# Kernel tuning notes

Hardware: AMD Instinct MI355X
Metric: run time of the kernel (lower is better)

## Reference

```python
import jax, jax.numpy as jnp
import numpy as np
import math

LN_EPS = 1e-5

def layer_norm(x, g, b):
    mu = jnp.mean(x, axis=-1, keepdims=True)
    var = jnp.mean(jnp.square(x - mu), axis=-1, keepdims=True)
    return (x - mu) * jax.lax.rsqrt(var + LN_EPS) * g + b

def positional_encoding(seq_len, d_model):
    pos = jnp.arange(seq_len, dtype=jnp.float32)[:, None]
    div = jnp.exp(jnp.arange(0, d_model, 2, dtype=jnp.float32) * (-math.log(10000.0) / d_model))
    ang = pos * div  # [S, D/2]
    # interleave: even indices sin, odd indices cos
    return jnp.stack([jnp.sin(ang), jnp.cos(ang)], axis=-1).reshape(seq_len, d_model)

def setup_inputs() -> dict:
    key = jax.random.key(0)
    V, D, H, L, F, B, S = 32000, 768, 12, 6, 3072, 4, 1024
    ks = jax.random.split(key, 12)
    s = 0.02
    inp = {
        'tokens': jax.random.randint(ks[0], (B, S), 0, V),
        'emb': jax.random.normal(ks[1], (V, D), jnp.float32) * s,
        'Wq': jax.random.normal(ks[2], (L, D, D), jnp.float32) * s,
        'bq': jnp.zeros((L, D), jnp.float32),
        'Wk': jax.random.normal(ks[3], (L, D, D), jnp.float32) * s,
        'bk': jnp.zeros((L, D), jnp.float32),
        'Wv': jax.random.normal(ks[4], (L, D, D), jnp.float32) * s,
        'bv': jnp.zeros((L, D), jnp.float32),
        'Wo': jax.random.normal(ks[5], (L, D, D), jnp.float32) * s,
        'bo': jnp.zeros((L, D), jnp.float32),
        'W1': jax.random.normal(ks[6], (L, D, F), jnp.float32) * s,
        'b1': jnp.zeros((L, F), jnp.float32),
        'W2': jax.random.normal(ks[7], (L, F, D), jnp.float32) * s,
        'b2': jnp.zeros((L, D), jnp.float32),
        'ln1_g': jnp.ones((L, D), jnp.float32), 'ln1_b': jnp.zeros((L, D), jnp.float32),
        'ln2_g': jnp.ones((L, D), jnp.float32), 'ln2_b': jnp.zeros((L, D), jnp.float32),
        'lnf_g': jnp.ones((D,), jnp.float32), 'lnf_b': jnp.zeros((D,), jnp.float32),
        'head_W': jax.random.normal(ks[8], (V, D), jnp.float32) * s,
    }
    return inp

def gpt_forward(tokens, emb, Wq, bq, Wk, bk, Wv, bv, Wo, bo, W1, b1, W2, b2,
                ln1_g, ln1_b, ln2_g, ln2_b, lnf_g, lnf_b, head_W):
    B, S = tokens.shape
    D = emb.shape[1]
    H = 12
    dk = D // H
    scale = 1.0 / math.sqrt(dk)
    causal = jnp.tril(jnp.ones((S, S), dtype=bool))  # [S,S]

    x = emb[tokens] + positional_encoding(S, D)  # [B,S,D]

    def block(x, p):
        wq, bq_, wk, bk_, wv, bv_, wo, bo_, w1, b1_, w2, b2_, g1, be1, g2, be2 = p
        h = layer_norm(x, g1, be1)
        q = (h @ wq + bq_).reshape(B, S, H, dk)
        k = (h @ wk + bk_).reshape(B, S, H, dk)
        v = (h @ wv + bv_).reshape(B, S, H, dk)
        scores = jnp.einsum('bqhd,bkhd->bhqk', q, k) * scale
        scores = jnp.where(causal, scores, -jnp.inf)
        attn = jax.nn.softmax(scores, axis=-1)
        o = jnp.einsum('bhqk,bkhd->bqhd', attn, v).reshape(B, S, D)
        x = x + o @ wo + bo_
        h2 = layer_norm(x, g2, be2)
        ff = jax.nn.gelu(h2 @ w1 + b1_, approximate=False) @ w2 + b2_
        x = x + ff
        return x, None

    layer_params = (Wq, bq, Wk, bk, Wv, bv, Wo, bo, W1, b1, W2, b2,
                    ln1_g, ln1_b, ln2_g, ln2_b)
    x, _ = jax.lax.scan(block, x, layer_params)
    x = layer_norm(x, lnf_g, lnf_b)
    logits = jnp.einsum('bsd,vd->bsv', x, head_W)  # head bias=False
    return logits

def reference(tokens, emb, Wq, bq, Wk, bk, Wv, bv, Wo, bo, W1, b1, W2, b2,
              ln1_g, ln1_b, ln2_g, ln2_b, lnf_g, lnf_b, head_W):
    return gpt_forward(tokens, emb, Wq, bq, Wk, bk, Wv, bv, Wo, bo, W1, b1, W2, b2,
                       ln1_g, ln1_b, ln2_g, ln2_b, lnf_g, lnf_b, head_W)
```

## Files before the change

kernel.cpp:

```cpp
#include <hip/hip_runtime.h>
#include <hip/hip_bf16.h>
#include <math.h>

#define BB 4
#define SS 1024
#define DD 768
#define HH 12
#define LL 6
#define FF 3072
#define VV 32000
#define DK 64
#define MM (BB * SS)

typedef __attribute__((ext_vector_type(8))) short s8v;
typedef __attribute__((ext_vector_type(4))) float f4v;

__device__ inline unsigned short f2bf_bits(float f) {
    unsigned u = __builtin_bit_cast(unsigned, f);
    unsigned r = (u + 0x7fffu + ((u >> 16) & 1u)) >> 16;
    return (unsigned short)r;
}

__device__ inline void gl_lds16(const void* g, void* l) {
    __builtin_amdgcn_global_load_lds((const __attribute__((address_space(1))) void*)g,
                                     (__attribute__((address_space(3))) void*)l, 16, 0, 0);
}

__global__ void embed_kernel(const int* __restrict__ tokens,
                             const float* __restrict__ emb,
                             float* __restrict__ x) {
    const int row = blockIdx.x;
    const int s = row % SS;
    const int tok = tokens[row];
    const float* er = emb + (size_t)tok * DD;
    float* xr = x + (size_t)row * DD;
    const float neg_ln_base = -logf(10000.0f) / (float)DD;
    for (int d = threadIdx.x; d < DD; d += blockDim.x) {
        int i2 = d & ~1;
        float div = expf((float)i2 * neg_ln_base);
        float ang = (float)s * div;
        float pe = (d & 1) ? cosf(ang) : sinf(ang);
        xr[d] = er[d] + pe;
    }
}

template <int OUTBF>
__global__ __launch_bounds__(256) void ln_kernel(const float* __restrict__ x,
                                                 const float* __restrict__ g,
                                                 const float* __restrict__ b,
                                                 void* __restrict__ outp) {
    const int row = blockIdx.x;
    const float* xr = x + (size_t)row * DD;
    float s = 0.f, s2 = 0.f;
    for (int d = threadIdx.x; d < DD; d += blockDim.x) {
        float v = xr[d];
        s += v; s2 += v * v;
    }
    __shared__ float rs[4], rs2[4];
    for (int off = 32; off; off >>= 1) {
        s  += __shfl_down(s, off);
        s2 += __shfl_down(s2, off);
    }
    const int wid = threadIdx.x >> 6;
    if ((threadIdx.x & 63) == 0) { rs[wid] = s; rs2[wid] = s2; }
    __syncthreads();
    s  = rs[0] + rs[1] + rs[2] + rs[3];
    s2 = rs2[0] + rs2[1] + rs2[2] + rs2[3];
    const float mu = s / (float)DD;
    const float var = s2 / (float)DD - mu * mu;
    const float r = rsqrtf(var + 1e-5f);
    for (int d = threadIdx.x; d < DD; d += blockDim.x) {
        float v = (xr[d] - mu) * r * g[d] + b[d];
        if (OUTBF) ((unsigned short*)outp)[(size_t)row * DD + d] = f2bf_bits(v);
        else       ((float*)outp)[(size_t)row * DD + d] = v;
    }
}

__global__ __launch_bounds__(256) void prep_kernel(const float* __restrict__ Wq,
                                                   const float* __restrict__ Wk,
                                                   const float* __restrict__ Wv,
                                                   const float* __restrict__ Wo,
                                                   const float* __restrict__ W1,
                                                   const float* __restrict__ W2,
                                                   unsigned short* __restrict__ wqkvT,
                                                   unsigned short* __restrict__ woT,
                                                   unsigned short* __restrict__ w1T,
                                                   unsigned short* __restrict__ w2T) {
    const size_t DxD = (size_t)DD * DD, DxF = (size_t)DD * FF;
    const int lid = blockIdx.x / 1728;
    const int id  = blockIdx.x % 1728;
    const float* src; unsigned short* dst; int R, C, t;
    if (id < 432)       { int seg = id / 144; t = id % 144;
                          src = (seg == 0 ? Wq : seg == 1 ? Wk : Wv) + lid * DxD;
                          dst = wqkvT + lid * 3 * DxD + (size_t)seg * DxD; R = DD; C = DD; }
    else if (id < 576)  { t = id - 432; src = Wo + lid * DxD; dst = woT + lid * DxD; R = DD; C = DD; }
    else if (id < 1152) { t = id - 576;  src = W1 + lid * DxF; dst = w1T + lid * DxF; R = DD; C = FF; }
    else                { t = id - 1152; src = W2 + lid * DxF; dst = w2T + lid * DxF; R = FF; C = DD; }
    const int tilesC = C / 64;
    const int r0 = (t / tilesC) * 64, c0 = (t % tilesC) * 64;
    __shared__ float tb[64][65];
    const int lr = threadIdx.x >> 6, lc = threadIdx.x & 63;
    #pragma unroll
    for (int it = 0; it < 16; ++it) {
        int r = it * 4 + lr;
        tb[r][lc] = src[(size_t)(r0 + r) * C + c0 + lc];
    }
    __syncthreads();
    #pragma unroll
    for (int it = 0; it < 16; ++it) {
        int c = it * 4 + lr;
        dst[(size_t)(c0 + c) * R + r0 + lc] = f2bf_bits(tb[lc][c]);
    }
}

__global__ __launch_bounds__(256) void conv_kernel(const float* __restrict__ in,
                                                   unsigned short* __restrict__ out,
                                                   long n4) {
    long i = (long)blockIdx.x * 256 + threadIdx.x;
    if (i < n4) {
        float4 v = ((const float4*)in)[i];
        ushort4 o;
        o.x = f2bf_bits(v.x); o.y = f2bf_bits(v.y);
        o.z = f2bf_bits(v.z); o.w = f2bf_bits(v.w);
        ((ushort4*)out)[i] = o;
    }
}

template <int BM, int BN, int WGM, int WGN, int ACT, int RES, int OUTMODE>
__global__ __launch_bounds__(256) void gemm_mfma(const unsigned short* __restrict__ A,
                                                 const unsigned short* __restrict__ Bt,
                                                 const float* __restrict__ bias,
                                                 const float* res,
                                                 void* Cout, int M, int N, int K,
                                                 const float* biasK, const float* biasV,
                                                 unsigned short* kout, unsigned short* vtout) {
    __shared__ unsigned short As[BM * 32];
    __shared__ unsigned short Bs[BN * 32];
    constexpr int MF = (BM / WGM) / 16;
    constexpr int NF = (BN / WGN) / 16;
    const int tid = threadIdx.x;
    const int bm = blockIdx.y * BM, bn = blockIdx.x * BN;
    const int lane = tid & 63;
    const int wave = tid >> 6;
    const int wr = (wave / WGN) * (BM / WGM);
    const int wc = (wave % WGN) * (BN / WGN);

    f4v acc[MF][NF];
    #pragma unroll
    for (int i = 0; i < MF; i++)
        #pragma unroll
        for (int j = 0; j < NF; j++)
            acc[i][j] = (f4v){0.f, 0.f, 0.f, 0.f};

    const int arow = tid >> 2;
    const int acol = (tid & 3) * 8;
    const int fr = lane & 15;
    const int fk = (lane >> 4) * 8;

    for (int k0 = 0; k0 < K; k0 += 32) {
        #pragma unroll
        for (int i = 0; i < BM / 64; i++)
            gl_lds16(A + (size_t)(bm + i * 64 + arow) * K + k0 + acol,
                     (char*)As + i * 4096 + tid * 16);
        #pragma unroll
        for (int i = 0; i < BN / 64; i++)
            gl_lds16(Bt + (size_t)(bn + i * 64 + arow) * K + k0 + acol,
                     (char*)Bs + i * 4096 + tid * 16);
        __syncthreads();
        s8v af[MF], bf[NF];
        #pragma unroll
        for (int i = 0; i < MF; i++)
            af[i] = *(const s8v*)(As + (wr + i * 16 + fr) * 32 + fk);
        #pragma unroll
        for (int j = 0; j < NF; j++)
            bf[j] = *(const s8v*)(Bs + (wc + j * 16 + fr) * 32 + fk);
        #pragma unroll
        for (int i = 0; i < MF; i++)
            #pragma unroll
            for (int j = 0; j < NF; j++)
                acc[i][j] = __builtin_amdgcn_mfma_f32_16x16x32_bf16(af[i], bf[j], acc[i][j], 0, 0, 0);
        __syncthreads();
    }

    const int r0 = bm + wr + (lane >> 4) * 4;
    const int c0 = bn + wc + fr;
    #pragma unroll
    for (int i = 0; i < MF; i++) {
        const int rb = r0 + i * 16;
        #pragma unroll
        for (int j = 0; j < NF; j++) {
            const int c = c0 + j * 16;
            if (OUTMODE == 3) {
                const int seg = (c >= 1536) ? 2 : (c >= 768 ? 1 : 0);
                const int cc = c - seg * 768;
                const float bb = (seg == 0 ? bias[cc] : seg == 1 ? biasK[cc] : biasV[cc]);
                if (seg < 2) {
                    unsigned short* dst = (seg == 0 ? (unsigned short*)Cout : kout);
                    #pragma unroll
                    for (int q = 0; q < 4; q++)
                        dst[(size_t)(rb + q) * DD + cc] = f2bf_bits(acc[i][j][q] + bb);
                } else {
                    const int b_ = rb / SS, s_ = rb % SS;
                    const int h_ = cc >> 6, dd = cc & 63;
                    ushort4 pk;
                    pk.x = f2bf_bits(acc[i][j][0] + bb);
                    pk.y = f2bf_bits(acc[i][j][1] + bb);
                    pk.z = f2bf_bits(acc[i][j][2] + bb);
                    pk.w = f2bf_bits(acc[i][j][3] + bb);
                    *(ushort4*)(vtout + ((size_t)(b_ * HH + h_) * DK + dd) * SS + s_) = pk;
                }
            } else {
                const float bv = bias ? bias[c] : 0.f;
                #pragma unroll
                for (int q = 0; q < 4; q++) {
                    const int r = rb + q;
                    float v = acc[i][j][q] + bv;
                    if (ACT) v = 0.5f * v * (1.0f + erff(v * 0.70710678118654752f));
                    if (RES) v += res[(size_t)r * N + c];
                    if (OUTMODE == 1) ((unsigned short*)Cout)[(size_t)r * N + c] = f2bf_bits(v);
                    else              ((float*)Cout)[(size_t)r * N + c] = v;
                }
            }
        }
    }
}

__global__ __launch_bounds__(512) void gemm_head(const unsigned short* __restrict__ A,
                                                 const unsigned short* __restrict__ Bt,
                                                 float* __restrict__ C,
                                                 int M, int N, int K) {
    __shared__ unsigned short As[256 * 32];
    __shared__ unsigned short Bs[128 * 32];
    const int tid = threadIdx.x;

    const int f = blockIdx.y * gridDim.x + blockIdx.x;
    const int v = (f & 7) * 500 + (f >> 3);
    int bx, by;
    if (v < 3840) {
        const int bnd = v >> 8;
        const int r = v & 255;
        by = r >> 4;
        bx = bnd * 16 + (r & 15);
    } else {
        const int r = v - 3840;
        by = r / 10;
        bx = 240 + r % 10;
    }
    const int bm = by * 256, bn = bx * 128;

    const int lane = tid & 63;
    const int wave = tid >> 6;
    const int wm = (wave >> 1) * 64;
    const int wn = (wave & 1) * 64;

    f4v acc[4][4];
    #pragma unroll
    for (int i = 0; i < 4; i++)
        #pragma unroll
        for (int j = 0; j < 4; j++)
            acc[i][j] = (f4v){0.f, 0.f, 0.f, 0.f};

    const int arow = tid >> 2;
    const int acol = (tid & 3) * 8;
    const unsigned short* gA0 = A  + (size_t)(bm + arow) * K + acol;
    const unsigned short* gA1 = gA0 + (size_t)128 * K;
    const unsigned short* gB  = Bt + (size_t)(bn + arow) * K + acol;
    char* lA0 = (char*)As + tid * 16;
    char* lA1 = lA0 + 8192;
    char* lB  = (char*)Bs + tid * 16;

    const int fr = lane & 15;
    const int fk = (lane >> 4) * 8;

    for (int k0 = 0; k0 < K; k0 += 32) {
        gl_lds16(gA0 + k0, lA0);
        gl_lds16(gA1 + k0, lA1);
        gl_lds16(gB + k0, lB);
        __syncthreads();
        s8v af[4], bf[4];
        #pragma unroll
        for (int i = 0; i < 4; i++)
            af[i] = *(const s8v*)(As + (wm + i * 16 + fr) * 32 + fk);
        #pragma unroll
        for (int j = 0; j < 4; j++)
            bf[j] = *(const s8v*)(Bs + (wn + j * 16 + fr) * 32 + fk);
        #pragma unroll
        for (int i = 0; i < 4; i++)
            #pragma unroll
            for (int j = 0; j < 4; j++)
                acc[i][j] = __builtin_amdgcn_mfma_f32_16x16x32_bf16(af[i], bf[j], acc[i][j], 0, 0, 0);
        __syncthreads();
    }

    const int r0 = bm + wm + (lane >> 4) * 4;
    const int c0 = bn + wn + fr;
    #pragma unroll
    for (int i = 0; i < 4; i++) {
        #pragma unroll
        for (int j = 0; j < 4; j++) {
            const int c = c0 + j * 16;
            #pragma unroll
            for (int q = 0; q < 4; q++) {
                const int r = r0 + i * 16 + q;
                __builtin_nontemporal_store(acc[i][j][q], &C[(size_t)r * N + c]);
            }
        }
    }
}

__global__ __launch_bounds__(256) void fattn_kernel(const unsigned short* __restrict__ qb,
                                                    const unsigned short* __restrict__ kb,
                                                    const unsigned short* __restrict__ vt,
                                                    unsigned short* __restrict__ o) {
    __shared__ unsigned short Ks[128 * 64];
    __shared__ unsigned short Vs[64 * 128];
    __shared__ unsigned short Ps[4][16 * 128];

    const int qt = (int)gridDim.x - 1 - (int)blockIdx.x;
    const int bh = blockIdx.y;
    const int b = bh / HH, h = bh % HH;
    const int tid = threadIdx.x;
    const int lane = tid & 63;
    const int w = tid >> 6;
    const int fr = lane & 15;
    const int g  = lane >> 4;

    const int krow_ = tid >> 3;
    const int kcol = ((tid & 7) ^ (krow_ & 7)) * 8;
    const int vrow_ = tid >> 4;
    const int vcol = ((tid & 15) ^ (vrow_ & 7)) * 8;

    const int q0w = qt * 64 + w * 16;
    s8v qf[2];
    {
        const unsigned short* qrow = qb + (size_t)(b * SS + q0w + fr) * DD + h * DK + g * 8;
        qf[0] = *(const s8v*)(qrow);
        qf[1] = *(const s8v*)(qrow + 32);
    }

    f4v ofr[4];
    #pragma unroll
    for (int dj = 0; dj < 4; dj++) ofr[dj] = (f4v){0.f, 0.f, 0.f, 0.f};
    float mrow[4] = {-1e30f, -1e30f, -1e30f, -1e30f};
    float lrow[4] = {0.f, 0.f, 0.f, 0.f};

    unsigned short* Pw = &Ps[w][0];
    const int ktiles = qt / 2 + 1;

    for (int t = 0; t < ktiles; ++t) {
        const int k0 = t * 128;
        #pragma unroll
        for (int i = 0; i < 4; i++) {
            const int r = i * 32 + krow_;
            gl_lds16(kb + (size_t)(b * SS + k0 + r) * DD + h * DK + kcol,
                     (char*)Ks + i * 4096 + tid * 16);
        }
        #pragma unroll
        for (int i = 0; i < 4; i++) {
            const int d = i * 16 + vrow_;
            gl_lds16(vt + ((size_t)bh * DK + d) * SS + k0 + vcol,
                     (char*)Vs + i * 4096 + tid * 16);
        }
        __syncthreads();

        const bool diag = (t == ktiles - 1);
        float p[8][4];
        #pragma unroll
        for (int j = 0; j < 8; j++) {
            const char* kbase = (const char*)Ks + (j * 16 + fr) * 128;
            s8v b0 = *(const s8v*)(kbase + ((g * 16)      ^ ((fr & 7) << 4)));
            s8v b1 = *(const s8v*)(kbase + ((64 + g * 16) ^ ((fr & 7) << 4)));
            f4v a = (f4v){0.f, 0.f, 0.f, 0.f};
            a = __builtin_amdgcn_mfma_f32_16x16x32_bf16(qf[0], b0, a, 0, 0, 0);
            a = __builtin_amdgcn_mfma_f32_16x16x32_bf16(qf[1], b1, a, 0, 0, 0);
            #pragma unroll
            for (int pq = 0; pq < 4; pq++) {
                float sv = a[pq] * 0.125f;
                if (diag && (k0 + j * 16 + fr > q0w + g * 4 + pq)) sv = -1e30f;
                p[j][pq] = sv;
            }
        }

        float rmx[4];
        #pragma unroll
        for (int pq = 0; pq < 4; pq++) {
            float v0 = fmaxf(fmaxf(p[0][pq], p[1][pq]), fmaxf(p[2][pq], p[3][pq]));
            float v1 = fmaxf(fmaxf(p[4][pq], p[5][pq]), fmaxf(p[6][pq], p[7][pq]));
            rmx[pq] = fmaxf(v0, v1);
        }
        #pragma unroll
        for (int off = 1; off < 16; off <<= 1)
            #pragma unroll
            for (int pq = 0; pq < 4; pq++)
                rmx[pq] = fmaxf(rmx[pq], __shfl_xor(rmx[pq], off));

        float mnew[4], scf[4], rsum[4];
        #pragma unroll
        for (int pq = 0; pq < 4; pq++) {
            mnew[pq] = fmaxf(mrow[pq], rmx[pq]);
            scf[pq]  = __expf(mrow[pq] - mnew[pq]);
            rsum[pq] = 0.f;
        }
        #pragma unroll
        for (int j = 0; j < 8; j++)
            #pragma unroll
            for (int pq = 0; pq < 4; pq++) {
                float e = __expf(p[j][pq] - mnew[pq]);
                p[j][pq] = e;
                rsum[pq] += e;
            }
        #pragma unroll
        for (int off = 1; off < 16; off <<= 1)
            #pragma unroll
            for (int pq = 0; pq < 4; pq++)
                rsum[pq] += __shfl_xor(rsum[pq], off);
        #pragma unroll
        for (int pq = 0; pq < 4; pq++) {
            lrow[pq] = lrow[pq] * scf[pq] + rsum[pq];
            mrow[pq] = mnew[pq];
        }
        #pragma unroll
        for (int dj = 0; dj < 4; dj++)
            #pragma unroll
            for (int pq = 0; pq < 4; pq++)
                ofr[dj][pq] *= scf[pq];

        #pragma unroll
        for (int j = 0; j < 8; j++)
            #pragma unroll
            for (int pq = 0; pq < 4; pq++) {
                const int r = g * 4 + pq;
                *(unsigned short*)((char*)Pw + r * 256 +
                                   (((j * 16 + fr) * 2) ^ ((r & 7) << 4))) = f2bf_bits(p[j][pq]);
            }

        s8v pa[4];
        #pragma unroll
        for (int ks = 0; ks < 4; ks++)
            pa[ks] = *(const s8v*)((const char*)Pw + fr * 256 +
                                   ((ks * 64 + g * 16) ^ ((fr & 7) << 4)));
        #pragma unroll
        for (int dj = 0; dj < 4; dj++) {
            const char* vbase = (const char*)Vs + (dj * 16 + fr) * 256;
            #pragma unroll
            for (int ks = 0; ks < 4; ks++) {
                s8v vv = *(const s8v*)(vbase + ((ks * 64 + g * 16) ^ ((fr & 7) << 4)));
                ofr[dj] = __builtin_amdgcn_mfma_f32_16x16x32_bf16(pa[ks], vv, ofr[dj], 0, 0, 0);
            }
        }
        __syncthreads();
    }

    #pragma unroll
    for (int pq = 0; pq < 4; pq++) {
        const float inv = 1.0f / lrow[pq];
        const int row_abs = q0w + g * 4 + pq;
        #pragma unroll
        for (int dj = 0; dj < 4; dj++)
            o[(size_t)(b * SS + row_abs) * DD + h * DK + dj * 16 + fr] =
                f2bf_bits(ofr[dj][pq] * inv);
    }
}

extern "C" void kernel_launch(void* const* d_in, const int* in_sizes, int n_in,
                              void* d_out, int out_size, void* d_ws, size_t ws_size,
                              hipStream_t stream) {
    const int*   tokens = (const int*)d_in[0];
    const float* emb    = (const float*)d_in[1];
    const float* Wq     = (const float*)d_in[2];
    const float* bq     = (const float*)d_in[3];
    const float* Wk     = (const float*)d_in[4];
    const float* bk     = (const float*)d_in[5];
    const float* Wv     = (const float*)d_in[6];
    const float* bv     = (const float*)d_in[7];
    const float* Wo     = (const float*)d_in[8];
    const float* bo     = (const float*)d_in[9];
    const float* W1     = (const float*)d_in[10];
    const float* b1     = (const float*)d_in[11];
    const float* W2     = (const float*)d_in[12];
    const float* b2     = (const float*)d_in[13];
    const float* ln1_g  = (const float*)d_in[14];
    const float* ln1_b  = (const float*)d_in[15];
    const float* ln2_g  = (const float*)d_in[16];
    const float* ln2_b  = (const float*)d_in[17];
    const float* lnf_g  = (const float*)d_in[18];
    const float* lnf_b  = (const float*)d_in[19];
    const float* headW  = (const float*)d_in[20];
    float* out = (float*)d_out;
    (void)in_sizes; (void)n_in; (void)out_size; (void)ws_size;

    const size_t MD  = (size_t)MM * DD;
    const size_t MF_ = (size_t)MM * FF;
    const size_t DxD = (size_t)DD * DD;
    const size_t DxF = (size_t)DD * FF;
    const size_t HWs = (size_t)VV * DD;

    char* p = (char*)d_ws;
    float*          x     = (float*)p;          p += MD * 4;
    unsigned short* qb    = (unsigned short*)p; p += MD * 2;
    unsigned short* kbuf  = (unsigned short*)p; p += MD * 2;
    unsigned short* vtb   = (unsigned short*)p; p += MD * 2;
    unsigned short* ao    = (unsigned short*)p; p += MD * 2;
    unsigned short* h     = (unsigned short*)p; p += MD * 2;
    unsigned short* mid   = (unsigned short*)p; p += MF_ * 2;
    unsigned short* wqkvT = (unsigned short*)p; p += 6 * 3 * DxD * 2;
    unsigned short* woT   = (unsigned short*)p; p += 6 * DxD * 2;
    unsigned short* w1T   = (unsigned short*)p; p += 6 * DxF * 2;
    unsigned short* w2T   = (unsigned short*)p; p += 6 * DxF * 2;
    unsigned short* hw    = (unsigned short*)p; p += HWs * 2;

    embed_kernel<<<MM, 256, 0, stream>>>(tokens, emb, x);
    conv_kernel<<<(int)((HWs / 4 + 255) / 256), 256, 0, stream>>>(headW, hw, (long)(HWs / 4));
    prep_kernel<<<6 * 1728, 256, 0, stream>>>(Wq, Wk, Wv, Wo, W1, W2, wqkvT, woT, w1T, w2T);

    const dim3 gQKV(2304 / 128, MM / 128);
    const dim3 gD(DD / 128, MM / 128);
    const dim3 gF(FF / 128, MM / 128);
    const dim3 gHead(VV / 128, MM / 256);
    const dim3 gA(SS / 64, BB * HH);

    for (int l = 0; l < LL; l++) {
        ln_kernel<1><<<MM, 256, 0, stream>>>(x, ln1_g + l * DD, ln1_b + l * DD, h);
        gemm_mfma<128, 128, 2, 2, 0, 0, 3><<<gQKV, 256, 0, stream>>>(
            h, wqkvT + (size_t)l * 3 * DxD, bq + l * DD, nullptr, qb, MM, 2304, DD,
            bk + l * DD, bv + l * DD, kbuf, vtb);
        fattn_kernel<<<gA, 256, 0, stream>>>(qb, kbuf, vtb, ao);
        gemm_mfma<128, 128, 2, 2, 0, 1, 0><<<gD, 256, 0, stream>>>(
            ao, woT + (size_t)l * DxD, bo + l * DD, x, x, MM, DD, DD,
            nullptr, nullptr, nullptr, nullptr);
        ln_kernel<1><<<MM, 256, 0, stream>>>(x, ln2_g + l * DD, ln2_b + l * DD, h);
        gemm_mfma<128, 128, 2, 2, 1, 0, 1><<<gF, 256, 0, stream>>>(
            h, w1T + (size_t)l * DxF, b1 + l * FF, nullptr, mid, MM, FF, DD,
            nullptr, nullptr, nullptr, nullptr);
        gemm_mfma<128, 128, 2, 2, 0, 1, 0><<<gD, 256, 0, stream>>>(
            mid, w2T + (size_t)l * DxF, b2 + l * DD, x, x, MM, DD, FF,
            nullptr, nullptr, nullptr, nullptr);
    }

    ln_kernel<1><<<MM, 256, 0, stream>>>(x, lnf_g, lnf_b, h);
    gemm_head<<<gHead, 512, 0, stream>>>(h, hw, out, MM, VV, DD);
}
```

Before: 1.861 ms.

## Rewrite LM-head GEMM with 256x256 tiles, double-buffered swizzled LDS pipeline

The vocabulary-projection GEMM moves from 256x128 tiles with a single K=32 LDS stage to 256x256 tiles that load K=64 per stage into two buffers. The LDS rows are XOR-swizzled to avoid bank conflicts. Async global-to-LDS prefetch of stage t+2 overlaps the MFMA work on the current stage, using explicit waitcnt, barriers and setprio. Each wave now holds 8x4 accumulators, which raises register pressure. The loop count of 12 is hardcoded, so the kernel assumes K=768.

```diff
diff --git a/kernel.cpp b/kernel.cpp
--- a/kernel.cpp
+++ b/kernel.cpp
@@ -225,77 +225,118 @@
     }
 }
 
-__global__ __launch_bounds__(512) void gemm_head(const unsigned short* __restrict__ A,
-                                                 const unsigned short* __restrict__ Bt,
-                                                 float* __restrict__ C,
-                                                 int M, int N, int K) {
-    __shared__ unsigned short As[256 * 32];
-    __shared__ unsigned short Bs[128 * 32];
+__global__ __launch_bounds__(512, 2) void gemm_head(const unsigned short* __restrict__ A,
+                                                    const unsigned short* __restrict__ Bt,
+                                                    float* __restrict__ C,
+                                                    int M, int N, int K) {
+    __shared__ unsigned short lds[2][2][256 * 64];
     const int tid = threadIdx.x;
-
-    const int f = blockIdx.y * gridDim.x + blockIdx.x;
-    const int v = (f & 7) * 500 + (f >> 3);
-    int bx, by;
-    if (v < 3840) {
-        const int bnd = v >> 8;
-        const int r = v & 255;
-        by = r >> 4;
-        bx = bnd * 16 + (r & 15);
-    } else {
-        const int r = v - 3840;
-        by = r / 10;
-        bx = 240 + r % 10;
-    }
-    const int bm = by * 256, bn = bx * 128;
-
     const int lane = tid & 63;
     const int wave = tid >> 6;
-    const int wm = (wave >> 1) * 64;
-    const int wn = (wave & 1) * 64;
-
-    f4v acc[4][4];
-    #pragma unroll
-    for (int i = 0; i < 4; i++)
+
+    const int f = blockIdx.y * gridDim.x + blockIdx.x;
+    const int v = (f & 7) * 250 + (f >> 3);
+    int bx, by;
+    if (v < 1920) { const int bnd = v >> 7; const int r = v & 127;
+                    by = r >> 3; bx = bnd * 8 + (r & 7); }
+    else          { const int r = v - 1920; by = r / 5; bx = 120 + r % 5; }
+    const int bm = by * 256, bn = bx * 256;
+
+    const int wr = (wave >> 2) * 128;
+    const int wc = (wave & 3) * 64;
+    const int fr = lane & 15;
+    const int g  = lane >> 4;
+
+    f4v acc[8][4];
+    #pragma unroll
+    for (int i = 0; i < 8; i++)
         #pragma unroll
         for (int j = 0; j < 4; j++)
             acc[i][j] = (f4v){0.f, 0.f, 0.f, 0.f};
 
-    const int arow = tid >> 2;
-    const int acol = (tid & 3) * 8;
-    const unsigned short* gA0 = A  + (size_t)(bm + arow) * K + acol;
-    const unsigned short* gA1 = gA0 + (size_t)128 * K;
-    const unsigned short* gB  = Bt + (size_t)(bn + arow) * K + acol;
-    char* lA0 = (char*)As + tid * 16;
-    char* lA1 = lA0 + 8192;
-    char* lB  = (char*)Bs + tid * 16;
-
-    const int fr = lane & 15;
-    const int fk = (lane >> 4) * 8;
-
-    for (int k0 = 0; k0 < K; k0 += 32) {
-        gl_lds16(gA0 + k0, lA0);
-        gl_lds16(gA1 + k0, lA1);
-        gl_lds16(gB + k0, lB);
-        __syncthreads();
-        s8v af[4], bf[4];
-        #pragma unroll
-        for (int i = 0; i < 4; i++)
-            af[i] = *(const s8v*)(As + (wm + i * 16 + fr) * 32 + fk);
-        #pragma unroll
-        for (int j = 0; j < 4; j++)
-            bf[j] = *(const s8v*)(Bs + (wn + j * 16 + fr) * 32 + fk);
-        #pragma unroll
-        for (int i = 0; i < 4; i++)
+    const int srow = tid >> 3;
+    const int schunk = tid & 7;
+    const int scsw = ((schunk ^ (srow & 7)) << 4);
+    const size_t kb = (size_t)K * 2;
+
+    const char* gA = (const char*)A  + (size_t)(bm + srow) * kb + scsw;
+    const char* gB = (const char*)Bt + (size_t)(bn + srow) * kb + scsw;
+    char* lA0 = (char*)(&lds[0][0][0]) + srow * 128 + (schunk << 4);
+    char* lB0 = (char*)(&lds[0][1][0]) + srow * 128 + (schunk << 4);
+
+#define HSTAGE(d, t)                                                          \
+    {                                                                         \
+        const size_t tk = (size_t)(t) * 128;                                  \
+        char* la = lA0 + (d) * 65536;                                         \
+        char* lb = lB0 + (d) * 65536;                                         \
+        _Pragma("unroll")                                                     \
+        for (int p = 0; p < 4; p++) {                                         \
+            gl_lds16(gA + (size_t)p * 64 * kb + tk, la + p * 64 * 128);       \
+            gl_lds16(gB + (size_t)p * 64 * kb + tk, lb + p * 64 * 128);       \
+        }                                                                     \
+    }
+
+    HSTAGE(0, 0);
+    HSTAGE(1, 1);
+    asm volatile("s_waitcnt vmcnt(8)" ::: "memory");
+    __builtin_amdgcn_sched_barrier(0);
+    __builtin_amdgcn_s_barrier();
+    __builtin_amdgcn_sched_barrier(0);
+
+    #pragma unroll 1
+    for (int t = 0; t < 12; ++t) {
+        const int cur = t & 1;
+        const char* baseA = (const char*)(&lds[cur][0][0]);
+        const char* baseB = (const char*)(&lds[cur][1][0]);
+
+        s8v bf[4][2], af[8][2];
+        #pragma unroll
+        for (int j = 0; j < 4; j++) {
+            const int row = wc + j * 16 + fr;
+            #pragma unroll
+            for (int ks = 0; ks < 2; ks++)
+                bf[j][ks] = *(const s8v*)(baseB + row * 128 +
+                                          ((ks * 64 + g * 16) ^ ((row & 7) << 4)));
+        }
+        #pragma unroll
+        for (int i = 0; i < 8; i++) {
+            const int row = wr + i * 16 + fr;
+            #pragma unroll
+            for (int ks = 0; ks < 2; ks++)
+                af[i][ks] = *(const s8v*)(baseA + row * 128 +
+                                          ((ks * 64 + g * 16) ^ ((row & 7) << 4)));
+        }
+
+        asm volatile("s_waitcnt lgkmcnt(0)" ::: "memory");
+        __builtin_amdgcn_sched_barrier(0);
+        __builtin_amdgcn_s_barrier();
+        __builtin_amdgcn_sched_barrier(0);
+
+        if (t + 2 < 12) HSTAGE(cur, t + 2);
+
+        __builtin_amdgcn_s_setprio(1);
+        #pragma unroll
+        for (int i = 0; i < 8; i++)
             #pragma unroll
             for (int j = 0; j < 4; j++)
-                acc[i][j] = __builtin_amdgcn_mfma_f32_16x16x32_bf16(af[i], bf[j], acc[i][j], 0, 0, 0);
-        __syncthreads();
-    }
-
-    const int r0 = bm + wm + (lane >> 4) * 4;
-    const int c0 = bn + wn + fr;
-    #pragma unroll
-    for (int i = 0; i < 4; i++) {
+                #pragma unroll
+                for (int ks = 0; ks < 2; ks++)
+                    acc[i][j] = __builtin_amdgcn_mfma_f32_16x16x32_bf16(
+                        af[i][ks], bf[j][ks], acc[i][j], 0, 0, 0);
+        __builtin_amdgcn_s_setprio(0);
+
+        if (t + 2 < 12) asm volatile("s_waitcnt vmcnt(8)" ::: "memory");
+        else            asm volatile("s_waitcnt vmcnt(0)" ::: "memory");
+        __builtin_amdgcn_sched_barrier(0);
+        __builtin_amdgcn_s_barrier();
+        __builtin_amdgcn_sched_barrier(0);
+    }
+#undef HSTAGE
+
+    const int r0 = bm + wr + g * 4;
+    const int c0 = bn + wc + fr;
+    #pragma unroll
+    for (int i = 0; i < 8; i++) {
         #pragma unroll
         for (int j = 0; j < 4; j++) {
             const int c = c0 + j * 16;
@@ -516,7 +557,7 @@
     const dim3 gQKV(2304 / 128, MM / 128);
     const dim3 gD(DD / 128, MM / 128);
     const dim3 gF(FF / 128, MM / 128);
-    const dim3 gHead(VV / 128, MM / 256);
+    const dim3 gHead(VV / 256, MM / 256);
     const dim3 gA(SS / 64, BB * HH);
 
     for (int l = 0; l < LL; l++) {
```

After: 1.881 ms. About the same (+1.1%).
